# Optimization experiments

Hardware: AMD Instinct MI355X
Metric: run time of the kernel (lower is better)

Reference implementation:

```python
import jax, jax.numpy as jnp
import numpy as np

H, D_MODEL, DK, DV = 16, 1024, 64, 64
B, S = 4, 2048
LN_EPS = 1e-6
NEG = -1e9


def setup_inputs() -> dict:
    key = jax.random.key(0)
    ks = jax.random.split(key, 8)
    query = jax.random.normal(ks[0], (B, S, D_MODEL), dtype=jnp.float32)
    k_in = jax.random.normal(ks[1], (B, S, D_MODEL), dtype=jnp.float32)
    v_in = jax.random.normal(ks[2], (B, S, D_MODEL), dtype=jnp.float32)
    mask = jax.random.randint(ks[3], (B, S, S), 0, 2, dtype=jnp.int32)
    sc = 1.0 / np.sqrt(D_MODEL)
    w_qs = jax.random.normal(ks[4], (D_MODEL, H * DK), dtype=jnp.float32) * sc
    w_ks = jax.random.normal(ks[5], (D_MODEL, H * DK), dtype=jnp.float32) * sc
    w_vs = jax.random.normal(ks[6], (D_MODEL, H * DV), dtype=jnp.float32) * sc
    w_out = jax.random.normal(ks[7], (H * DV, D_MODEL), dtype=jnp.float32) * (1.0 / np.sqrt(H * DV))
    ln_g = jnp.ones((D_MODEL,), dtype=jnp.float32)
    ln_b = jnp.zeros((D_MODEL,), dtype=jnp.float32)
    return {"query": query, "key": k_in, "value": v_in, "mask": mask,
            "w_qs": w_qs, "w_ks": w_ks, "w_vs": w_vs, "w_out": w_out,
            "ln_g": ln_g, "ln_b": ln_b}


def reference(query, key, value, mask, w_qs, w_ks, w_vs, w_out, ln_g, ln_b):
    # projections -> [B, H, S, dk/dv]
    q = (query @ w_qs).reshape(B, S, H, DK).transpose(0, 2, 1, 3)
    k = (key @ w_ks).reshape(B, S, H, DK).transpose(0, 2, 1, 3)
    v = (value @ w_vs).reshape(B, S, H, DV).transpose(0, 2, 1, 3)
    scores = jnp.einsum('bhqd,bhkd->bhqk', q, k) / np.sqrt(DK)
    scores = jnp.where(mask[:, None, :, :] == 0, NEG, scores)
    p = jax.nn.softmax(scores, axis=-1)  # dropout = identity in eval
    x = jnp.einsum('bhqk,bhkd->bhqd', p, v)  # [B,H,S,DV]
    x = x.transpose(0, 2, 1, 3).reshape(B, S, H * DV)
    out = x @ w_out + query  # dropout identity, residual
    mu = out.mean(-1, keepdims=True)
    var = out.var(-1, keepdims=True)
    return (out - mu) / jnp.sqrt(var + LN_EPS) * ln_g + ln_b
```

## Files before the change

kernel.cpp:

```cpp
#include <hip/hip_runtime.h>

#define BB   4
#define SS   2048
#define HH   16
#define DM   1024
#define DKV  64
#define LNEPS 1e-6f

#define MD_BF16 0
#define MD_F32  1
#define MD_F16  2

typedef __attribute__((ext_vector_type(8))) short bf16x8;
typedef __attribute__((ext_vector_type(4))) float f32x4;
#define MFMA16(a,b,c) __builtin_amdgcn_mfma_f32_16x16x32_bf16(a,b,c,0,0,0)

__device__ __forceinline__ void gl_lds16(const ushort* g, ushort* l) {
    __builtin_amdgcn_global_load_lds(
        (const __attribute__((address_space(1))) void*)g,
        (__attribute__((address_space(3))) void*)l, 16, 0, 0);
}
__device__ __forceinline__ void wait_vm0_barrier() {
    asm volatile("s_waitcnt vmcnt(0)" ::: "memory");
    __builtin_amdgcn_s_barrier();
}

__device__ __forceinline__ float2 unpack2(unsigned int u) {
    union { unsigned int i; float f; } a, b;
    a.i = u << 16;
    b.i = u & 0xffff0000u;
    return make_float2(a.f, b.f);
}
__device__ __forceinline__ unsigned short f2bf(float f) {
    union { float f; unsigned int i; } c; c.f = f;
    unsigned int u = c.i;
    unsigned int r = u + 0x7fffu + ((u >> 16) & 1u);
    return (unsigned short)(r >> 16);
}
__device__ __forceinline__ unsigned short f2bf_t(float f) {
    union { float f; unsigned int i; } c; c.f = f;
    return (unsigned short)(c.i >> 16);
}
__device__ __forceinline__ float h2f(unsigned int bits16) {
    unsigned short s = (unsigned short)bits16;
    _Float16 x;
    __builtin_memcpy(&x, &s, 2);
    return (float)x;
}
__device__ __forceinline__ void load4m(const void* p, int mode, size_t e0, float* o) {
    if (mode == MD_F32) {
        float4 v = *(const float4*)((const float*)p + e0);
        o[0] = v.x; o[1] = v.y; o[2] = v.z; o[3] = v.w;
    } else {
        uint2 u = *(const uint2*)((const ushort*)p + e0);
        if (mode == MD_BF16) {
            float2 a = unpack2(u.x), b = unpack2(u.y);
            o[0] = a.x; o[1] = a.y; o[2] = b.x; o[3] = b.y;
        } else {
            o[0] = h2f(u.x & 0xFFFFu); o[1] = h2f(u.x >> 16);
            o[2] = h2f(u.y & 0xFFFFu); o[3] = h2f(u.y >> 16);
        }
    }
}
__device__ __forceinline__ float loadS(const void* p, int mode, size_t i) {
    if (mode == MD_F32) return ((const float*)p)[i];
    unsigned short u = ((const ushort*)p)[i];
    if (mode == MD_BF16) { union { unsigned i; float f; } c; c.i = (unsigned)u << 16; return c.f; }
    return h2f(u);
}

__device__ __forceinline__ void loadAraw(const void* p, int m, size_t e, uint4* r) {
    if (m == MD_F32) {
        const float* f = (const float*)p + e;
        r[0] = *(const uint4*)(f);
        r[1] = *(const uint4*)(f + 4);
        r[2] = *(const uint4*)(f + 8);
        r[3] = *(const uint4*)(f + 12);
    } else {
        const ushort* s = (const ushort*)p + e;
        r[0] = *(const uint4*)s;
        r[1] = *(const uint4*)(s + 8);
    }
}
__device__ __forceinline__ void cvtA16(const uint4* r, int m, uint4* o2) {
    union { ushort u[16]; uint4 v[2]; } o;
    if (m == MD_F32) {
        const float* f = (const float*)r;
#pragma unroll
        for (int j = 0; j < 16; ++j) o.u[j] = f2bf(f[j]);
    } else if (m == MD_BF16) {
        o.v[0] = r[0]; o.v[1] = r[1];
    } else {
        const ushort* s = (const ushort*)r;
#pragma unroll
        for (int j = 0; j < 16; ++j) o.u[j] = f2bf(h2f(s[j]));
    }
    o2[0] = o.v[0]; o2[1] = o.v[1];
}

__device__ __forceinline__ int sniff_local(const void* p_, int nhalf) {
    __shared__ int cE, cO;
    const ushort* p = (const ushort*)p_;
    if (threadIdx.x == 0) { cE = 0; cO = 0; }
    __syncthreads();
    int e = 0, o = 0;
    for (int i = threadIdx.x; i < nhalf; i += 256) {
        unsigned ex = (p[i] >> 7) & 0xFFu;
        int hit = (ex < 100u || ex == 0xFFu) ? 1 : 0;
        if (i & 1) o += hit; else e += hit;
    }
    atomicAdd(&cE, e);
    atomicAdd(&cO, o);
    __syncthreads();
    const int total = cE + cO;
    return (total < 48) ? MD_BF16 : ((cO * 4 < cE) ? MD_F32 : MD_F16);
}

__device__ __forceinline__ void wtrans_body(
    const void* __restrict__ W, ushort* __restrict__ Wt, int m, int sub)
{
    __shared__ ushort T[64][68];
    const int tid = threadIdx.x;
    const int n0 = (sub & 15) * 64, k0 = (sub >> 4) * 64;

    const int r = tid >> 2, c = (tid & 3) * 16;
    float t[4];
#pragma unroll
    for (int j = 0; j < 4; ++j) {
        load4m(W, m, (size_t)(k0 + r) * DM + n0 + c + 4 * j, t);
#pragma unroll
        for (int i = 0; i < 4; ++i) T[r][c + 4 * j + i] = f2bf(t[i]);
    }
    __syncthreads();

    const int rn = tid >> 2, ck = (tid & 3) * 16;
    union { ushort u[8]; uint4 v; } p0, p1;
#pragma unroll
    for (int j = 0; j < 8; ++j) { p0.u[j] = T[ck + j][rn]; p1.u[j] = T[ck + 8 + j][rn]; }
    ushort* op = &Wt[(size_t)(n0 + rn) * DM + k0 + ck];
    *(uint4*)op = p0.v;
    *(uint4*)(op + 8) = p1.v;
}

__device__ __forceinline__ void aconv_body(
    const void* __restrict__ A, ushort* __restrict__ Ab, int bidl)
{
    const int m = sniff_local(A, 4096);
    const size_t e0 = ((size_t)bidl * 256 + threadIdx.x) * 16;
    uint4 r[4], o[2];
    loadAraw(A, m, e0, r);
    cvtA16(r, m, o);
    *(uint4*)&Ab[e0]     = o[0];
    *(uint4*)&Ab[e0 + 8] = o[1];
}

__global__ __launch_bounds__(256) void prep(
    const int* __restrict__ mask, unsigned int* __restrict__ pm,
    const void* __restrict__ w_qs, const void* __restrict__ w_ks,
    const void* __restrict__ w_vs, const void* __restrict__ w_out,
    ushort* __restrict__ Wtq, ushort* __restrict__ Wtk,
    ushort* __restrict__ Wtv, ushort* __restrict__ Wt2,
    const void* __restrict__ query, const void* __restrict__ value,
    ushort* __restrict__ Abq, ushort* __restrict__ Abv)
{
    const int bid = blockIdx.x;
    if (bid < 2048) {
        const int w = bid * 256 + threadIdx.x;
        const int* p = mask + (size_t)w * 32;
        unsigned int bits = 0u;
#pragma unroll
        for (int j = 0; j < 8; ++j) {
            int4 v = *(const int4*)(p + j * 4);
            bits |= (v.x ? 1u : 0u) << (4 * j);
            bits |= (v.y ? 1u : 0u) << (4 * j + 1);
            bits |= (v.z ? 1u : 0u) << (4 * j + 2);
            bits |= (v.w ? 1u : 0u) << (4 * j + 3);
        }
        pm[w] = bits;
    } else if (bid < 3072) {
        const int b2 = bid - 2048;
        const int g = b2 >> 8, sub = b2 & 255;
        const void* W = (g == 0) ? w_qs : (g == 1) ? w_ks : (g == 2) ? w_vs : w_out;
        ushort* Wt = (g == 0) ? Wtq : (g == 1) ? Wtk : (g == 2) ? Wtv : Wt2;
        wtrans_body(W, Wt, sniff_local(W, 4096), sub);
    } else if (bid < 5120) {
        aconv_body(query, Abq, bid - 3072);
    } else {
        aconv_body(value, Abv, bid - 5120);
    }
}

__global__ __launch_bounds__(256) void aconv_k(
    const void* __restrict__ A, ushort* __restrict__ Ab)
{
    aconv_body(A, Ab, blockIdx.x);
}

struct ProjArgs {
    const ushort* A[2]; const ushort* Wt[2]; ushort* Out[2];
    int vmode[2]; float scale[2];
};

__global__ __launch_bounds__(256) void proj_mfma(ProjArgs pa)
{
    __shared__ __align__(16) ushort Asf[2][4096];
    __shared__ __align__(16) ushort Bsf[2][4096];

    const int z = blockIdx.z;
    const ushort* A  = pa.A[z];
    const ushort* Wt = pa.Wt[z];
    ushort* Out = pa.Out[z];
    const int vmode = pa.vmode[z];
    const float scale = pa.scale[z];

    const int tid = threadIdx.x;
    const int lane = tid & 63, wv = tid >> 6;
    const int quad = lane >> 4, L = lane & 15;
    const int bid = blockIdx.y * gridDim.x + blockIdx.x;
    const int swz = (bid & 7) * 64 + (bid >> 3);
    const int m0 = (swz >> 3) * 128, n0 = (swz & 7) * 128;
    const int wm = (wv >> 1) * 64, wn = (wv & 1) * 64;

    const int e0 = (wv * 2 + 0) * 512 + lane * 8;
    const int e1 = (wv * 2 + 1) * 512 + lane * 8;
    const ushort* gA0 = A  + (size_t)(m0 + (e0 >> 5)) * DM + (e0 & 31);
    const ushort* gA1 = A  + (size_t)(m0 + (e1 >> 5)) * DM + (e1 & 31);
    const ushort* gB0 = Wt + (size_t)(n0 + (e0 >> 5)) * DM + (e0 & 31);
    const ushort* gB1 = Wt + (size_t)(n0 + (e1 >> 5)) * DM + (e1 & 31);

    f32x4 acc[4][4];
#pragma unroll
    for (int i = 0; i < 4; ++i)
#pragma unroll
        for (int j = 0; j < 4; ++j) { acc[i][j][0] = 0.f; acc[i][j][1] = 0.f; acc[i][j][2] = 0.f; acc[i][j][3] = 0.f; }

    gl_lds16(gA0, &Asf[0][e0]);
    gl_lds16(gA1, &Asf[0][e1]);
    gl_lds16(gB0, &Bsf[0][e0]);
    gl_lds16(gB1, &Bsf[0][e1]);
    wait_vm0_barrier();

    int cur = 0;
    for (int kt = 0; kt < 31; ++kt) {
        const int kn = (kt + 1) * 32;
        gl_lds16(gA0 + kn, &Asf[cur ^ 1][e0]);
        gl_lds16(gA1 + kn, &Asf[cur ^ 1][e1]);
        gl_lds16(gB0 + kn, &Bsf[cur ^ 1][e0]);
        gl_lds16(gB1 + kn, &Bsf[cur ^ 1][e1]);

        bf16x8 af[4], bfr[4];
#pragma unroll
        for (int tm = 0; tm < 4; ++tm) af[tm] = *(const bf16x8*)&Asf[cur][(wm + tm * 16 + L) * 32 + quad * 8];
#pragma unroll
        for (int tn = 0; tn < 4; ++tn) bfr[tn] = *(const bf16x8*)&Bsf[cur][(wn + tn * 16 + L) * 32 + quad * 8];
#pragma unroll
        for (int tm = 0; tm < 4; ++tm)
#pragma unroll
            for (int tn = 0; tn < 4; ++tn)
                acc[tm][tn] = MFMA16(af[tm], bfr[tn], acc[tm][tn]);

        wait_vm0_barrier();
        cur ^= 1;
    }
    {
        bf16x8 af[4], bfr[4];
#pragma unroll
        for (int tm = 0; tm < 4; ++tm) af[tm] = *(const bf16x8*)&Asf[cur][(wm + tm * 16 + L) * 32 + quad * 8];
#pragma unroll
        for (int tn = 0; tn < 4; ++tn) bfr[tn] = *(const bf16x8*)&Bsf[cur][(wn + tn * 16 + L) * 32 + quad * 8];
#pragma unroll
        for (int tm = 0; tm < 4; ++tm)
#pragma unroll
            for (int tn = 0; tn < 4; ++tn)
                acc[tm][tn] = MFMA16(af[tm], bfr[tn], acc[tm][tn]);
    }

#pragma unroll
    for (int tm = 0; tm < 4; ++tm)
#pragma unroll
        for (int tn = 0; tn < 4; ++tn)
#pragma unroll
            for (int r = 0; r < 4; ++r) {
                const int mm = m0 + wm + tm * 16 + quad * 4 + r;
                const int n = n0 + wn + tn * 16 + L;
                const int b = mm >> 11, s = mm & 2047;
                const int h = n >> 6, d = n & 63;
                const size_t o = vmode
                    ? ((size_t)(b * HH + h) * DKV + d) * SS + s
                    : ((size_t)(b * HH + h) * SS + s) * DKV + d;
                Out[o] = f2bf(acc[tm][tn][r] * scale);
            }
}

__global__ __launch_bounds__(256) void attn_mfma(
    const ushort* __restrict__ Q, const ushort* __restrict__ K,
    const ushort* __restrict__ Vt, const unsigned int* __restrict__ pm,
    ushort* __restrict__ Xo)
{
    __shared__ __align__(16) ushort Ks[64][72];
    __shared__ __align__(16) ushort Vs[64][72];
    __shared__ __align__(16) ushort Ps[64][72];

    const int tid = threadIdx.x;
    const int lane = tid & 63, wv = tid >> 6;
    const int quad = lane >> 4, L = lane & 15;
    const int bid = blockIdx.y * gridDim.x + blockIdx.x;
    const int swz = (bid & 7) * 256 + (bid >> 3);
    const int bh = swz >> 5, b = bh >> 4, h = bh & 15;
    const int q0 = (swz & 31) * 64;

    const ushort* qp = &Q[((size_t)bh * SS + q0 + wv * 16 + L) * DKV + quad * 8];
    const bf16x8 aq0 = *(const bf16x8*)qp;
    const bf16x8 aq1 = *(const bf16x8*)(qp + 32);

    f32x4 O[4];
    float lacc[4];
#pragma unroll
    for (int t = 0; t < 4; ++t) { O[t][0] = 0.f; O[t][1] = 0.f; O[t][2] = 0.f; O[t][3] = 0.f; }
#pragma unroll
    for (int r = 0; r < 4; ++r) lacc[r] = 0.f;

    const int sr = tid >> 2, sg = tid & 3;
    const ushort* kbase = &K[((size_t)bh * SS + sr) * DKV + sg * 16];
    const ushort* vbase = &Vt[((size_t)bh * DKV + sr) * SS + sg * 16];
    const unsigned int* pmr[4];
#pragma unroll
    for (int r = 0; r < 4; ++r)
        pmr[r] = pm + ((size_t)b * SS + q0 + wv * 16 + quad * 4 + r) * 64;

    for (int kt = 0; kt < 32; ++kt) {
        uint2 mw[4];
#pragma unroll
        for (int r = 0; r < 4; ++r) mw[r] = *(const uint2*)(pmr[r] + 2 * kt);

        __syncthreads();
        *(uint4*)&Ks[sr][sg * 16]     = *(const uint4*)kbase;
        *(uint4*)&Ks[sr][sg * 16 + 8] = *(const uint4*)(kbase + 8);
        *(uint4*)&Vs[sr][sg * 16]     = *(const uint4*)vbase;
        *(uint4*)&Vs[sr][sg * 16 + 8] = *(const uint4*)(vbase + 8);
        kbase += 64 * DKV;
        vbase += 64;
        __syncthreads();

        f32x4 sc[4];
        __builtin_amdgcn_s_setprio(1);
#pragma unroll
        for (int t = 0; t < 4; ++t) {
            bf16x8 b0 = *(const bf16x8*)&Ks[t * 16 + L][quad * 8];
            bf16x8 b1 = *(const bf16x8*)&Ks[t * 16 + L][32 + quad * 8];
            f32x4 c; c[0] = 0.f; c[1] = 0.f; c[2] = 0.f; c[3] = 0.f;
            c = MFMA16(aq0, b0, c);
            c = MFMA16(aq1, b1, c);
            sc[t] = c;
        }
        __builtin_amdgcn_s_setprio(0);

#pragma unroll
        for (int r = 0; r < 4; ++r) {
            const unsigned mx = mw[r].x, my = mw[r].y;
#pragma unroll
            for (int t = 0; t < 4; ++t) {
                const float s = fminf(sc[t][r], 30.f);
                const float e = __expf(s);
                const unsigned wsel = (t & 2) ? my : mx;
                const float p = ((wsel >> ((t & 1) * 16 + L)) & 1u) ? e : 0.f;
                lacc[r] += p;
                Ps[wv * 16 + quad * 4 + r][t * 16 + L] = f2bf_t(p);
            }
        }

        bf16x8 ap0 = *(const bf16x8*)&Ps[wv * 16 + L][quad * 8];
        bf16x8 ap1 = *(const bf16x8*)&Ps[wv * 16 + L][32 + quad * 8];
        __builtin_amdgcn_s_setprio(1);
#pragma unroll
        for (int t = 0; t < 4; ++t) {
            bf16x8 v0 = *(const bf16x8*)&Vs[t * 16 + L][quad * 8];
            bf16x8 v1 = *(const bf16x8*)&Vs[t * 16 + L][32 + quad * 8];
            O[t] = MFMA16(ap0, v0, O[t]);
            O[t] = MFMA16(ap1, v1, O[t]);
        }
        __builtin_amdgcn_s_setprio(0);
    }

    float inv[4];
#pragma unroll
    for (int r = 0; r < 4; ++r) {
        float l = lacc[r];
#pragma unroll
        for (int off = 1; off < 16; off <<= 1) l += __shfl_xor(l, off, 64);
        inv[r] = 1.f / l;
    }
#pragma unroll
    for (int t = 0; t < 4; ++t)
#pragma unroll
        for (int r = 0; r < 4; ++r) {
            const int qg = q0 + wv * 16 + quad * 4 + r;
            Xo[((size_t)b * SS + qg) * DM + h * DKV + t * 16 + L] = f2bf(O[t][r] * inv[r]);
        }
}

__global__ __launch_bounds__(256) void oproj_mfma(
    const ushort* __restrict__ Xin, const ushort* __restrict__ Wt,
    const void* __restrict__ Qres, float* __restrict__ OutF)
{
    __shared__ __align__(16) ushort Asf[2][4096];
    __shared__ __align__(16) ushort Bsf[2][4096];

    const int mq = sniff_local(Qres, 4096);

    const int tid = threadIdx.x;
    const int lane = tid & 63, wv = tid >> 6;
    const int quad = lane >> 4, L = lane & 15;
    const int bid = blockIdx.y * gridDim.x + blockIdx.x;
    const int swz = (bid & 7) * 64 + (bid >> 3);
    const int m0 = (swz >> 3) * 128, n0 = (swz & 7) * 128;
    const int wm = (wv >> 1) * 64, wn = (wv & 1) * 64;

    const int e0 = (wv * 2 + 0) * 512 + lane * 8;
    const int e1 = (wv * 2 + 1) * 512 + lane * 8;
    const ushort* gA0 = Xin + (size_t)(m0 + (e0 >> 5)) * DM + (e0 & 31);
    const ushort* gA1 = Xin + (size_t)(m0 + (e1 >> 5)) * DM + (e1 & 31);
    const ushort* gB0 = Wt  + (size_t)(n0 + (e0 >> 5)) * DM + (e0 & 31);
    const ushort* gB1 = Wt  + (size_t)(n0 + (e1 >> 5)) * DM + (e1 & 31);

    f32x4 acc[4][4];
#pragma unroll
    for (int i = 0; i < 4; ++i)
#pragma unroll
        for (int j = 0; j < 4; ++j) { acc[i][j][0] = 0.f; acc[i][j][1] = 0.f; acc[i][j][2] = 0.f; acc[i][j][3] = 0.f; }

    gl_lds16(gA0, &Asf[0][e0]);
    gl_lds16(gA1, &Asf[0][e1]);
    gl_lds16(gB0, &Bsf[0][e0]);
    gl_lds16(gB1, &Bsf[0][e1]);
    wait_vm0_barrier();

    int cur = 0;
    for (int kt = 0; kt < 31; ++kt) {
        const int kn = (kt + 1) * 32;
        gl_lds16(gA0 + kn, &Asf[cur ^ 1][e0]);
        gl_lds16(gA1 + kn, &Asf[cur ^ 1][e1]);
        gl_lds16(gB0 + kn, &Bsf[cur ^ 1][e0]);
        gl_lds16(gB1 + kn, &Bsf[cur ^ 1][e1]);

        bf16x8 af[4], bfr[4];
#pragma unroll
        for (int tm = 0; tm < 4; ++tm) af[tm] = *(const bf16x8*)&Asf[cur][(wm + tm * 16 + L) * 32 + quad * 8];
#pragma unroll
        for (int tn = 0; tn < 4; ++tn) bfr[tn] = *(const bf16x8*)&Bsf[cur][(wn + tn * 16 + L) * 32 + quad * 8];
#pragma unroll
        for (int tm = 0; tm < 4; ++tm)
#pragma unroll
            for (int tn = 0; tn < 4; ++tn)
                acc[tm][tn] = MFMA16(af[tm], bfr[tn], acc[tm][tn]);

        wait_vm0_barrier();
        cur ^= 1;
    }
    {
        bf16x8 af[4], bfr[4];
#pragma unroll
        for (int tm = 0; tm < 4; ++tm) af[tm] = *(const bf16x8*)&Asf[cur][(wm + tm * 16 + L) * 32 + quad * 8];
#pragma unroll
        for (int tn = 0; tn < 4; ++tn) bfr[tn] = *(const bf16x8*)&Bsf[cur][(wn + tn * 16 + L) * 32 + quad * 8];
#pragma unroll
        for (int tm = 0; tm < 4; ++tm)
#pragma unroll
            for (int tn = 0; tn < 4; ++tn)
                acc[tm][tn] = MFMA16(af[tm], bfr[tn], acc[tm][tn]);
    }

#pragma unroll
    for (int tm = 0; tm < 4; ++tm)
#pragma unroll
        for (int tn = 0; tn < 4; ++tn)
#pragma unroll
            for (int r = 0; r < 4; ++r) {
                const int mm = m0 + wm + tm * 16 + quad * 4 + r;
                const int n = n0 + wn + tn * 16 + L;
                const size_t idx = (size_t)mm * DM + n;
                OutF[idx] = acc[tm][tn][r] + loadS(Qres, mq, idx);
            }
}

__global__ __launch_bounds__(256) void ln_k(
    const float* __restrict__ In, float* __restrict__ Out,
    const void* __restrict__ G, const void* __restrict__ Bt)
{
    const int mg = sniff_local(G, 1024);
    const int mb = sniff_local(Bt, 1024);

    const int tid = threadIdx.x, wv = tid >> 6, lane = tid & 63;
    const int row = blockIdx.x * 4 + wv;
    const size_t base = (size_t)row * DM + lane * 16;

    float v[16];
    float s = 0.f, q = 0.f;
#pragma unroll
    for (int j = 0; j < 16; j += 4) {
        float4 t = *(const float4*)&In[base + j];
        v[j] = t.x; v[j+1] = t.y; v[j+2] = t.z; v[j+3] = t.w;
        s += t.x + t.y + t.z + t.w;
        q += t.x*t.x + t.y*t.y + t.z*t.z + t.w*t.w;
    }
#pragma unroll
    for (int off = 1; off < 64; off <<= 1) {
        s += __shfl_xor(s, off, 64);
        q += __shfl_xor(q, off, 64);
    }
    const float mu = s * (1.f / 1024.f);
    const float var = q * (1.f / 1024.f) - mu * mu;
    const float inv = rsqrtf(var + LNEPS);

    float gj[16], bj[16];
#pragma unroll
    for (int j = 0; j < 16; j += 4) {
        load4m(G,  mg, (size_t)lane * 16 + j, gj + j);
        load4m(Bt, mb, (size_t)lane * 16 + j, bj + j);
    }
#pragma unroll
    for (int j = 0; j < 16; j += 4) {
        float4 o;
        o.x = (v[j]   - mu) * inv * gj[j]   + bj[j];
        o.y = (v[j+1] - mu) * inv * gj[j+1] + bj[j+1];
        o.z = (v[j+2] - mu) * inv * gj[j+2] + bj[j+2];
        o.w = (v[j+3] - mu) * inv * gj[j+3] + bj[j+3];
        *(float4*)&Out[base + j] = o;
    }
}

extern "C" void kernel_launch(void* const* d_in, const int* in_sizes, int n_in,
                              void* d_out, int out_size, void* d_ws, size_t ws_size,
                              hipStream_t stream)
{
    const void* query = d_in[0];
    const void* key_i = d_in[1];
    const void* value = d_in[2];
    const int*  mask  = (const int*)d_in[3];
    const void* w_qs  = d_in[4];
    const void* w_ks  = d_in[5];
    const void* w_vs  = d_in[6];
    const void* w_out = d_in[7];
    const void* ln_g  = d_in[8];
    const void* ln_b  = d_in[9];
    float* out = (float*)d_out;

    const size_t PE = (size_t)BB * HH * SS * DKV;
    ushort* Qw = (ushort*)((char*)d_ws + 256);
    ushort* Kw = Qw + PE;
    ushort* Vw = Kw + PE;
    ushort* Xw = Vw + PE;
    float*  OutF = (float*)Qw;
    unsigned int* pmask = (unsigned int*)d_out;
    ushort* Wtq = (ushort*)((char*)d_out + (2 << 20));
    ushort* Wtk = (ushort*)((char*)d_out + (4 << 20));
    ushort* Wtv = (ushort*)((char*)d_out + (6 << 20));
    ushort* Wt2 = (ushort*)((char*)d_out + (8 << 20));
    ushort* Abq = (ushort*)((char*)d_out + (10 << 20));
    ushort* Abv = Xw;
    ushort* Abk = Xw;

    prep<<<7168, 256, 0, stream>>>(mask, pmask, w_qs, w_ks, w_vs, w_out,
                                   Wtq, Wtk, Wtv, Wt2, query, value, Abq, Abv);

    ProjArgs pqv;
    pqv.A[0] = Abq; pqv.Wt[0] = Wtq; pqv.Out[0] = Qw; pqv.vmode[0] = 0; pqv.scale[0] = 0.125f;
    pqv.A[1] = Abv; pqv.Wt[1] = Wtv; pqv.Out[1] = Vw; pqv.vmode[1] = 1; pqv.scale[1] = 1.0f;
    proj_mfma<<<dim3(8, 64, 2), 256, 0, stream>>>(pqv);

    aconv_k<<<2048, 256, 0, stream>>>(key_i, Abk);

    ProjArgs pk;
    pk.A[0] = Abk; pk.Wt[0] = Wtk; pk.Out[0] = Kw; pk.vmode[0] = 0; pk.scale[0] = 1.0f;
    pk.A[1] = Abk; pk.Wt[1] = Wtk; pk.Out[1] = Kw; pk.vmode[1] = 0; pk.scale[1] = 1.0f;
    proj_mfma<<<dim3(8, 64, 1), 256, 0, stream>>>(pk);

    attn_mfma<<<dim3(32, 64), 256, 0, stream>>>(Qw, Kw, Vw, pmask, Xw);

    oproj_mfma<<<dim3(8, 64), 256, 0, stream>>>(Xw, Wt2, query, OutF);

    ln_k<<<2048, 256, 0, stream>>>(OutF, out, ln_g, ln_b);
}
```

Before: 542.1 us.

## Stage V-projection epilogue through LDS for coalesced transposed stores; swizzle P tile

The projection kernel's shared buffers are merged into one array so that, for the transposed V output, the accumulator tile can be written into LDS and then stored as contiguous 16-byte rows along the sequence dimension. This replaces scattered 2-byte strided writes to global memory. The attention kernel also XOR-swizzles the P tile's column index on write and read, aiming to cut LDS bank conflicts. The costs are extra barriers and LDS traffic in the V epilogue, and the swizzle must match exactly between writer and reader.

```diff
diff --git a/kernel.cpp b/kernel.cpp
--- a/kernel.cpp
+++ b/kernel.cpp
@@ -201,10 +201,12 @@
     int vmode[2]; float scale[2];
 };
 
+#define ASF(BUF) (SMEM + (BUF) * 4096)
+#define BSF(BUF) (SMEM + 8192 + (BUF) * 4096)
+
 __global__ __launch_bounds__(256) void proj_mfma(ProjArgs pa)
 {
-    __shared__ __align__(16) ushort Asf[2][4096];
-    __shared__ __align__(16) ushort Bsf[2][4096];
+    __shared__ __align__(16) ushort SMEM[17408];
 
     const int z = blockIdx.z;
     const ushort* A  = pa.A[z];
@@ -234,25 +236,25 @@
 #pragma unroll
         for (int j = 0; j < 4; ++j) { acc[i][j][0] = 0.f; acc[i][j][1] = 0.f; acc[i][j][2] = 0.f; acc[i][j][3] = 0.f; }
 
-    gl_lds16(gA0, &Asf[0][e0]);
-    gl_lds16(gA1, &Asf[0][e1]);
-    gl_lds16(gB0, &Bsf[0][e0]);
-    gl_lds16(gB1, &Bsf[0][e1]);
+    gl_lds16(gA0, ASF(0) + e0);
+    gl_lds16(gA1, ASF(0) + e1);
+    gl_lds16(gB0, BSF(0) + e0);
+    gl_lds16(gB1, BSF(0) + e1);
     wait_vm0_barrier();
 
     int cur = 0;
     for (int kt = 0; kt < 31; ++kt) {
         const int kn = (kt + 1) * 32;
-        gl_lds16(gA0 + kn, &Asf[cur ^ 1][e0]);
-        gl_lds16(gA1 + kn, &Asf[cur ^ 1][e1]);
-        gl_lds16(gB0 + kn, &Bsf[cur ^ 1][e0]);
-        gl_lds16(gB1 + kn, &Bsf[cur ^ 1][e1]);
+        gl_lds16(gA0 + kn, ASF(cur ^ 1) + e0);
+        gl_lds16(gA1 + kn, ASF(cur ^ 1) + e1);
+        gl_lds16(gB0 + kn, BSF(cur ^ 1) + e0);
+        gl_lds16(gB1 + kn, BSF(cur ^ 1) + e1);
 
         bf16x8 af[4], bfr[4];
 #pragma unroll
-        for (int tm = 0; tm < 4; ++tm) af[tm] = *(const bf16x8*)&Asf[cur][(wm + tm * 16 + L) * 32 + quad * 8];
-#pragma unroll
-        for (int tn = 0; tn < 4; ++tn) bfr[tn] = *(const bf16x8*)&Bsf[cur][(wn + tn * 16 + L) * 32 + quad * 8];
+        for (int tm = 0; tm < 4; ++tm) af[tm] = *(const bf16x8*)(ASF(cur) + (wm + tm * 16 + L) * 32 + quad * 8);
+#pragma unroll
+        for (int tn = 0; tn < 4; ++tn) bfr[tn] = *(const bf16x8*)(BSF(cur) + (wn + tn * 16 + L) * 32 + quad * 8);
 #pragma unroll
         for (int tm = 0; tm < 4; ++tm)
 #pragma unroll
@@ -265,9 +267,9 @@
     {
         bf16x8 af[4], bfr[4];
 #pragma unroll
-        for (int tm = 0; tm < 4; ++tm) af[tm] = *(const bf16x8*)&Asf[cur][(wm + tm * 16 + L) * 32 + quad * 8];
-#pragma unroll
-        for (int tn = 0; tn < 4; ++tn) bfr[tn] = *(const bf16x8*)&Bsf[cur][(wn + tn * 16 + L) * 32 + quad * 8];
+        for (int tm = 0; tm < 4; ++tm) af[tm] = *(const bf16x8*)(ASF(cur) + (wm + tm * 16 + L) * 32 + quad * 8);
+#pragma unroll
+        for (int tn = 0; tn < 4; ++tn) bfr[tn] = *(const bf16x8*)(BSF(cur) + (wn + tn * 16 + L) * 32 + quad * 8);
 #pragma unroll
         for (int tm = 0; tm < 4; ++tm)
 #pragma unroll
@@ -275,21 +277,43 @@
                 acc[tm][tn] = MFMA16(af[tm], bfr[tn], acc[tm][tn]);
     }
 
-#pragma unroll
-    for (int tm = 0; tm < 4; ++tm)
-#pragma unroll
-        for (int tn = 0; tn < 4; ++tn)
-#pragma unroll
-            for (int r = 0; r < 4; ++r) {
-                const int mm = m0 + wm + tm * 16 + quad * 4 + r;
-                const int n = n0 + wn + tn * 16 + L;
-                const int b = mm >> 11, s = mm & 2047;
-                const int h = n >> 6, d = n & 63;
-                const size_t o = vmode
-                    ? ((size_t)(b * HH + h) * DKV + d) * SS + s
-                    : ((size_t)(b * HH + h) * SS + s) * DKV + d;
-                Out[o] = f2bf(acc[tm][tn][r] * scale);
-            }
+    if (!vmode) {
+#pragma unroll
+        for (int tm = 0; tm < 4; ++tm)
+#pragma unroll
+            for (int tn = 0; tn < 4; ++tn)
+#pragma unroll
+                for (int r = 0; r < 4; ++r) {
+                    const int mm = m0 + wm + tm * 16 + quad * 4 + r;
+                    const int n = n0 + wn + tn * 16 + L;
+                    const int b = mm >> 11, s = mm & 2047;
+                    const int h = n >> 6, d = n & 63;
+                    Out[((size_t)(b * HH + h) * SS + s) * DKV + d] =
+                        f2bf(acc[tm][tn][r] * scale);
+                }
+    } else {
+        __syncthreads();
+        ushort (*T)[136] = (ushort (*)[136])SMEM;
+#pragma unroll
+        for (int tm = 0; tm < 4; ++tm)
+#pragma unroll
+            for (int tn = 0; tn < 4; ++tn)
+#pragma unroll
+                for (int r = 0; r < 4; ++r)
+                    T[wn + tn * 16 + L][wm + tm * 16 + quad * 4 + r] =
+                        f2bf(acc[tm][tn][r] * scale);
+        __syncthreads();
+
+        const int row = tid >> 1, half = tid & 1;
+        const int ng = n0 + row;
+        const int h = ng >> 6, d = ng & 63;
+        const int b = m0 >> 11, s0v = m0 & 2047;
+        ushort* dst = Out + ((size_t)(b * HH + h) * DKV + d) * SS + s0v + half * 64;
+        const ushort* srcT = &T[row][half * 64];
+#pragma unroll
+        for (int j = 0; j < 8; ++j)
+            *(uint4*)(dst + j * 8) = *(const uint4*)(srcT + j * 8);
+    }
 }
 
 __global__ __launch_bounds__(256) void attn_mfma(
@@ -327,6 +351,9 @@
 #pragma unroll
     for (int r = 0; r < 4; ++r)
         pmr[r] = pm + ((size_t)b * SS + q0 + wv * 16 + quad * 4 + r) * 64;
+
+    const int wsw = quad << 3;
+    const int fr  = ((L >> 2) & 3) << 3;
 
     for (int kt = 0; kt < 32; ++kt) {
         uint2 mw[4];
@@ -365,12 +392,12 @@
                 const unsigned wsel = (t & 2) ? my : mx;
                 const float p = ((wsel >> ((t & 1) * 16 + L)) & 1u) ? e : 0.f;
                 lacc[r] += p;
-                Ps[wv * 16 + quad * 4 + r][t * 16 + L] = f2bf_t(p);
+                Ps[wv * 16 + quad * 4 + r][(t * 16 + L) ^ wsw] = f2bf_t(p);
             }
         }
 
-        bf16x8 ap0 = *(const bf16x8*)&Ps[wv * 16 + L][quad * 8];
-        bf16x8 ap1 = *(const bf16x8*)&Ps[wv * 16 + L][32 + quad * 8];
+        bf16x8 ap0 = *(const bf16x8*)&Ps[wv * 16 + L][(quad * 8) ^ fr];
+        bf16x8 ap1 = *(const bf16x8*)&Ps[wv * 16 + L][32 + ((quad * 8) ^ fr)];
         __builtin_amdgcn_s_setprio(1);
 #pragma unroll
         for (int t = 0; t < 4; ++t) {
```

Result: no change. 532.1 us (-1.8%).
